# Performance work log

Hardware: AMD Instinct MI355X
Metric: run time of the kernel (lower is better)

The kernel has to match this reference:

```python
import jax, jax.numpy as jnp
import numpy as np

B, T, D, H = 2, 2048, 1024, 16
Dh = D // H
V = 32000  # vocab for kWTA potentials
KW_DECAY, KW_THR, K_WIN = 0.7, 1.0, 5
GAIN_UP, GAIN_DOWN = 1.5, 0.6
SPIKE_THR = 0.5


def setup_inputs() -> dict:
    key = jax.random.key(0)
    ks = jax.random.split(key, 10)
    x = jax.random.normal(ks[0], (B, T, D), dtype=jnp.float32)
    token_ids = jax.random.randint(ks[1], (B, T), 0, V)
    # xavier_uniform with gain 0.5 for square DxD weights
    bound = 0.5 * np.sqrt(6.0 / (D + D))
    def w(k):
        return jax.random.uniform(k, (D, D), dtype=jnp.float32, minval=-bound, maxval=bound)
    Wr, Wk, Wv, Wo = w(ks[2]), w(ks[3]), w(ks[4]), w(ks[5])
    bo = jnp.zeros((D,), dtype=jnp.float32)
    def tm(k):
        return jax.random.uniform(k, (1, 1, D), dtype=jnp.float32, minval=0.1, maxval=0.9)
    time_mix_k, time_mix_v, time_mix_r = tm(ks[6]), tm(ks[7]), tm(ks[8])
    return {"x": x, "token_ids": token_ids, "Wr": Wr, "Wk": Wk, "Wv": Wv,
            "Wo": Wo, "bo": bo, "time_mix_k": time_mix_k,
            "time_mix_v": time_mix_v, "time_mix_r": time_mix_r}


def kwta_gains(token_ids):
    """Sequential spiking k-WTA over the flattened token stream -> (V,) gains."""
    ids = token_ids.reshape(-1)
    def step(carry, tid):
        pot, spk = carry
        pot = pot * KW_DECAY
        pot = pot.at[tid].add(1.0)          # bincount of single token
        fired = pot >= KW_THR
        spk = spk + fired.astype(jnp.int32)
        pot = jnp.where(fired, pot - KW_THR, pot)  # soft reset
        return (pot, spk), None
    init = (jnp.zeros((V,), jnp.float32), jnp.zeros((V,), jnp.int32))
    (pot, spk), _ = jax.lax.scan(step, init, ids)
    values = spk.astype(jnp.float32) * 1e6 + pot
    topk_idx = jax.lax.top_k(values, K_WIN)[1]
    gains = jnp.where(spk > 0, GAIN_DOWN, 1.0).astype(jnp.float32)
    gains = gains.at[topk_idx].set(GAIN_UP)
    return gains


def spike_activation(x):
    # training-mode STE: hard spikes forward, clamp(1-|x-thr|,0,1) surrogate grad
    spikes = (x > SPIKE_THR).astype(x.dtype)
    ste = jnp.clip(1.0 - jnp.abs(x - SPIKE_THR), 0.0, 1.0)
    return spikes + ste - jax.lax.stop_gradient(ste)


def reference(x, token_ids, Wr, Wk, Wv, Wo, bo, time_mix_k, time_mix_v, time_mix_r):
    gains = jax.lax.stop_gradient(kwta_gains(token_ids))[:D]  # (D,)
    # token shift: prev_state starts as zeros
    prev_x = jnp.concatenate([jnp.zeros((B, 1, D), x.dtype), x[:, :-1]], axis=1)
    def mix(tm):
        m = tm.reshape(D) * gains               # adaptive time mixing with kWTA gains
        return m * x + (1.0 - m) * prev_x
    xr, xk, xv = mix(time_mix_r), mix(time_mix_k), mix(time_mix_v)
    r = xr @ Wr.T                                # [B,T,D]
    k = spike_activation(xk @ Wk.T)
    v = xv @ Wv.T
    def heads(t):
        return t.reshape(B, T, H, Dh).transpose(0, 2, 1, 3)  # [B,H,T,Dh]
    q_, k_, v_ = heads(r), heads(k), heads(v)
    # chunked_attention is an exact tiled full (non-causal) softmax attention
    scores = jnp.einsum('bhqd,bhkd->bhqk', q_, k_) * (1.0 / np.sqrt(Dh))
    attn = jax.nn.softmax(scores, axis=-1)
    out = jnp.einsum('bhqk,bhkd->bhqd', attn, v_)
    out = out.transpose(0, 2, 1, 3).reshape(B, T, D)
    out = jax.nn.sigmoid(r) * out                # receptance gating
    return out @ Wo.T + bo
```

## Files before the change

### kernel.cpp

```cpp
#include <hip/hip_runtime.h>
#include <stdint.h>

static constexpr int CB = 2, CT = 2048, CD = 1024, CH = 16, CDh = 64, CV = 32000;
static constexpr int CM = CB * CT;

typedef float f32x4 __attribute__((ext_vector_type(4)));
typedef float f32x16 __attribute__((ext_vector_type(16)));
typedef short s16x8 __attribute__((ext_vector_type(8)));
typedef unsigned u32x2 __attribute__((ext_vector_type(2)));

__device__ __forceinline__ unsigned short f2bf(float f) {
  unsigned u = __builtin_bit_cast(unsigned, f);
  unsigned r = 0x7FFFu + ((u >> 16) & 1u);
  return (unsigned short)((u + r) >> 16);
}
__device__ __forceinline__ float bf2f(unsigned short h) {
  unsigned u = ((unsigned)h) << 16;
  return __builtin_bit_cast(float, u);
}
__device__ __forceinline__ unsigned pkrh(float a, float b) {
  unsigned ua = __builtin_bit_cast(unsigned, a) + 0x8000u;
  unsigned ub = __builtin_bit_cast(unsigned, b) + 0x8000u;
  return __builtin_amdgcn_perm(ub, ua, 0x07060302);
}
__device__ __forceinline__ void lds_cp16(const void* g, void* l) {
  __builtin_amdgcn_global_load_lds(
      (const __attribute__((address_space(1))) unsigned*)g,
      (__attribute__((address_space(3))) unsigned*)l, 16, 0, 0);
}

__device__ __forceinline__ void chain5(unsigned n, unsigned& b0, unsigned& b1, unsigned& b2,
                                       unsigned& b3, unsigned& b4) {
  unsigned t;
  t = b0 > n ? b0 : n; n = b0 > n ? n : b0; b0 = t;
  t = b1 > n ? b1 : n; n = b1 > n ? n : b1; b1 = t;
  t = b2 > n ? b2 : n; n = b2 > n ? n : b2; b2 = t;
  t = b3 > n ? b3 : n; n = b3 > n ? n : b3; b3 = t;
  b4 = b4 > n ? b4 : n;
}

__global__ __launch_bounds__(1024) void nsr_gains(const int* __restrict__ ids,
                                                  int* __restrict__ bins,
                                                  float* __restrict__ gains) {
  __shared__ unsigned l5[5120];
  __shared__ unsigned w5[320];
  __shared__ unsigned fin[5];
  int tid = threadIdx.x;
  for (int i = tid; i < CV; i += 1024) bins[i] = 0;
  __syncthreads();
#pragma unroll
  for (int i = 0; i < 4; ++i) atomicAdd(&bins[ids[i * 1024 + tid]], 1);
  __syncthreads();
  unsigned b0 = 0, b1 = 0, b2 = 0, b3 = 0, b4 = 0;
  for (int i = tid; i < CV; i += 1024) {
    unsigned key = (((unsigned)bins[i]) << 15) | (unsigned)(32767 - i);
    chain5(key, b0, b1, b2, b3, b4);
  }
  l5[tid] = b0; l5[1024 + tid] = b1; l5[2048 + tid] = b2; l5[3072 + tid] = b3; l5[4096 + tid] = b4;
  __syncthreads();
  if (tid < 64) {
    unsigned c0 = 0, c1 = 0, c2 = 0, c3 = 0, c4 = 0;
    for (int i = tid; i < 5120; i += 64) chain5(l5[i], c0, c1, c2, c3, c4);
    w5[tid] = c0; w5[64 + tid] = c1; w5[128 + tid] = c2; w5[192 + tid] = c3; w5[256 + tid] = c4;
  }
  __syncthreads();
  if (tid == 0) {
    unsigned c0 = 0, c1 = 0, c2 = 0, c3 = 0, c4 = 0;
    for (int i = 0; i < 320; ++i) chain5(w5[i], c0, c1, c2, c3, c4);
    fin[0] = c0; fin[1] = c1; fin[2] = c2; fin[3] = c3; fin[4] = c4;
  }
  __syncthreads();
  {
    int cnt = bins[tid];
    float g = cnt > 0 ? 0.6f : 1.0f;
    unsigned key = (((unsigned)cnt) << 15) | (unsigned)(32767 - tid);
    if (key == fin[0] || key == fin[1] || key == fin[2] || key == fin[3] || key == fin[4])
      g = 1.5f;
    gains[tid] = g;
  }
}

__device__ __forceinline__ unsigned short mix1(float tm, float g, float xc, float px) {
  float m = tm * g;
  return f2bf(m * xc + (1.f - m) * px);
}

__global__ void nsr_cvtw_mix(const float* __restrict__ Wr, const float* __restrict__ Wk,
                             const float* __restrict__ Wv, const float* __restrict__ Wo,
                             unsigned short* __restrict__ dst, const float* __restrict__ x,
                             const float* __restrict__ gains, const float* __restrict__ tmr,
                             const float* __restrict__ tmk, const float* __restrict__ tmv,
                             unsigned short* __restrict__ xr, unsigned short* __restrict__ xk,
                             unsigned short* __restrict__ xv) {
  int bid = blockIdx.x;
  if (bid < 4096) {
    int i = bid * 256 + threadIdx.x;
    int which = i >> 18;
    int j = (i & 0x3FFFF) << 2;
    const float* s = which == 0 ? Wr : which == 1 ? Wk : which == 2 ? Wv : Wo;
    float4 v = *(const float4*)(s + j);
    ushort4 o = make_ushort4(f2bf(v.x), f2bf(v.y), f2bf(v.z), f2bf(v.w));
    *(ushort4*)(dst + (size_t)which * (CD * CD) + j) = o;
  } else {
    int i = (bid - 4096) * 256 + threadIdx.x;
    int m = i >> 8;
    int d = (i & 255) << 2;
    int t = m & (CT - 1);
    size_t base = (size_t)m * CD + d;
    float4 xc = *(const float4*)(x + base);
    float4 px = make_float4(0.f, 0.f, 0.f, 0.f);
    if (t > 0) px = *(const float4*)(x + base - CD);
    float4 g = *(const float4*)(gains + d);
    float4 ar = *(const float4*)(tmr + d);
    float4 ak = *(const float4*)(tmk + d);
    float4 av = *(const float4*)(tmv + d);
    *(ushort4*)(xr + base) = make_ushort4(mix1(ar.x, g.x, xc.x, px.x), mix1(ar.y, g.y, xc.y, px.y),
                                          mix1(ar.z, g.z, xc.z, px.z), mix1(ar.w, g.w, xc.w, px.w));
    *(ushort4*)(xk + base) = make_ushort4(mix1(ak.x, g.x, xc.x, px.x), mix1(ak.y, g.y, xc.y, px.y),
                                          mix1(ak.z, g.z, xc.z, px.z), mix1(ak.w, g.w, xc.w, px.w));
    *(ushort4*)(xv + base) = make_ushort4(mix1(av.x, g.x, xc.x, px.x), mix1(av.y, g.y, xc.y, px.y),
                                          mix1(av.z, g.z, xc.z, px.z), mix1(av.w, g.w, xc.w, px.w));
  }
}

__device__ __forceinline__ void swz_tiles(int bl, int& m0, int& n0) {
  int xcd = bl & 7, idx = bl >> 3;
  int mt8 = xcd * 4 + (idx & 3);
  int nt8 = idx >> 2;
  m0 = mt8 << 7;
  n0 = nt8 << 7;
}

__device__ __forceinline__ void gemm128(const unsigned short* __restrict__ A,
                                        const unsigned short* __restrict__ W, int m0, int n0,
                                        int Klen, int ld, int tid, f32x4 acc[4][4],
                                        unsigned short* As, unsigned short* Bs) {
  const f32x4 fz = {0.f, 0.f, 0.f, 0.f};
  int lane = tid & 63, w = tid >> 6;
  int wm = (w >> 1) << 6, wn = (w & 1) << 6;
  int l15 = lane & 15, quad = lane >> 4;
#pragma unroll
  for (int mt = 0; mt < 4; ++mt)
#pragma unroll
    for (int nt = 0; nt < 4; ++nt) acc[mt][nt] = fz;
  for (int k0 = 0; k0 < Klen; k0 += 32) {
#pragma unroll
    for (int i = 0; i < 2; ++i) {
      int chunk = i * 256 + tid;
      int r = chunk >> 2, cp = chunk & 3, c = cp ^ (r & 3);
      lds_cp16(A + (size_t)(m0 + r) * ld + k0 + c * 8, &As[(chunk & ~63) << 3]);
      lds_cp16(W + (size_t)(n0 + r) * ld + k0 + c * 8, &Bs[(chunk & ~63) << 3]);
    }
    __syncthreads();
    s16x8 af[4], bf[4];
#pragma unroll
    for (int mt = 0; mt < 4; ++mt) {
      int row = wm + mt * 16 + l15;
      af[mt] = *(const s16x8*)&As[row * 32 + ((quad ^ (row & 3)) << 3)];
    }
#pragma unroll
    for (int nt = 0; nt < 4; ++nt) {
      int row = wn + nt * 16 + l15;
      bf[nt] = *(const s16x8*)&Bs[row * 32 + ((quad ^ (row & 3)) << 3)];
    }
#pragma unroll
    for (int mt = 0; mt < 4; ++mt)
#pragma unroll
      for (int nt = 0; nt < 4; ++nt)
        acc[mt][nt] = __builtin_amdgcn_mfma_f32_16x16x32_bf16(af[mt], bf[nt], acc[mt][nt], 0, 0, 0);
    __syncthreads();
  }
}

__global__ __launch_bounds__(256) void nsr_proj(const unsigned short* __restrict__ xr,
                                                const unsigned short* __restrict__ xk,
                                                const unsigned short* __restrict__ xv,
                                                const unsigned short* __restrict__ Wb,
                                                unsigned short* __restrict__ r,
                                                unsigned short* __restrict__ k,
                                                unsigned short* __restrict__ vt) {
  __shared__ alignas(16) unsigned short As[128 * 32];
  __shared__ alignas(16) unsigned short Bs[128 * 32];
  __shared__ alignas(16) unsigned short vts[128 * 136];
  int bid = blockIdx.x;
  int which = bid >> 8;
  int m0, n0;
  swz_tiles(bid & 255, m0, n0);
  const unsigned short* A = which == 0 ? xr : which == 1 ? xk : xv;
  const unsigned short* W = Wb + (size_t)which * (CD * CD);
  f32x4 acc[4][4];
  gemm128(A, W, m0, n0, CD, CD, threadIdx.x, acc, As, Bs);
  int tid = threadIdx.x;
  int lane = tid & 63, w = tid >> 6;
  int wm = (w >> 1) << 6, wn = (w & 1) << 6;
  int l15 = lane & 15, quad = lane >> 4;
  if (which < 2) {
    unsigned short* out = which == 0 ? r : k;
#pragma unroll
    for (int mt = 0; mt < 4; ++mt)
#pragma unroll
      for (int nt = 0; nt < 4; ++nt)
#pragma unroll
        for (int rr = 0; rr < 4; ++rr) {
          int grow = m0 + wm + mt * 16 + quad * 4 + rr;
          int gcol = n0 + wn + nt * 16 + l15;
          float val = acc[mt][nt][rr];
          if (which == 1) val = val > 0.5f ? 1.0f : 0.0f;
          out[(size_t)grow * CD + gcol] = f2bf(val);
        }
  } else {
#pragma unroll
    for (int mt = 0; mt < 4; ++mt)
#pragma unroll
      for (int nt = 0; nt < 4; ++nt) {
        int gcl = wn + nt * 16 + l15;
        int gr = wm + mt * 16 + quad * 4;
        unsigned lo = pkrh(acc[mt][nt][0], acc[mt][nt][1]);
        unsigned hi = pkrh(acc[mt][nt][2], acc[mt][nt][3]);
        uint2 pk = make_uint2(lo, hi);
        *(uint2*)&vts[gcl * 136 + gr] = pk;
      }
    __syncthreads();
    int b2 = m0 >> 11, t0 = m0 & (CT - 1);
    int ch = tid & 15, dl2 = tid >> 4;
#pragma unroll
    for (int rr2 = 0; rr2 < 8; ++rr2) {
      int dloc = rr2 * 16 + dl2;
      int h = (n0 + dloc) >> 6, dl = (n0 + dloc) & 63;
      s16x8 val = *(const s16x8*)&vts[dloc * 136 + ch * 8];
      size_t ob = ((size_t)((b2 * CH + h) * CDh + dl)) * CT + t0 + ch * 8;
      *(s16x8*)(vt + ob) = val;
    }
  }
}

__global__ __launch_bounds__(512, 2) void nsr_attn(const unsigned short* __restrict__ rbf,
                                                   const unsigned short* __restrict__ kbf,
                                                   const unsigned short* __restrict__ vt,
                                                   unsigned short* __restrict__ gated) {
  __shared__ alignas(16) unsigned char smem[32768];
  __shared__ float denp[2][128];
  unsigned short* Ks = (unsigned short*)smem;
  unsigned short* Vs = (unsigned short*)(smem + 16384);
  float* Ored = (float*)smem;

  const f32x16 fz16 = {0.f, 0.f, 0.f, 0.f, 0.f, 0.f, 0.f, 0.f,
                       0.f, 0.f, 0.f, 0.f, 0.f, 0.f, 0.f, 0.f};
  const float EXSC = 0.125f * 1.44269504088896f;
  int bid = blockIdx.x;
  int b = bid & 1, hd = (bid >> 1) & 15, qt = bid >> 5;
  int tid = threadIdx.x, lane = tid & 63, w = tid >> 6;
  int l31 = lane & 31, hbit = lane >> 5;
  int qh = w & 3, kq2 = w >> 2;

  const unsigned short* qrow = rbf + (size_t)(b * CT + qt * 128 + qh * 32 + l31) * CD + hd * 64;
  s16x8 qfrag[4];
#pragma unroll
  for (int s4 = 0; s4 < 4; ++s4) {
    s16x8 qf = *(const s16x8*)(qrow + s4 * 16 + hbit * 8);
    unsigned* qd = (unsigned*)&qf;
#pragma unroll
    for (int j = 0; j < 4; ++j) {
      float lo = __builtin_bit_cast(float, qd[j] << 16) * EXSC;
      float hi = __builtin_bit_cast(float, qd[j] & 0xFFFF0000u) * EXSC;
      qd[j] = pkrh(lo, hi);
    }
    qfrag[s4] = qf;
  }

  const unsigned short* kap[2][4];
#pragma unroll
  for (int ktile = 0; ktile < 2; ++ktile) {
    int keyrow = kq2 * 64 + ktile * 32 + l31;
#pragma unroll
    for (int s4 = 0; s4 < 4; ++s4) {
      int cp = (s4 * 2 + hbit) ^ (keyrow & 7);
      kap[ktile][s4] = &Ks[keyrow * 64 + cp * 8];
    }
  }
  const unsigned short* vap[2][2][2];
#pragma unroll
  for (int ktile = 0; ktile < 2; ++ktile)
#pragma unroll
    for (int s = 0; s < 2; ++s)
#pragma unroll
      for (int dt = 0; dt < 2; ++dt) {
        int drow = dt * 32 + l31;
        int c = kq2 * 8 + ktile * 4 + s * 2 + hbit;
        int cp = (c & 8) | ((c ^ drow) & 7);
        vap[ktile][s][dt] = &Vs[drow * 128 + cp * 8];
      }

  const unsigned short* kgp[2];
  const unsigned short* vgp[2];
  unsigned short* ldk[2];
  unsigned short* ldv[2];
  {
    const unsigned short* kgbase = kbf + (size_t)(b * CT) * CD + hd * 64;
    const unsigned short* vgbase = vt + (size_t)((b * CH + hd) * CDh) * CT;
#pragma unroll
    for (int i = 0; i < 2; ++i) {
      int L = i * 512 + tid;
      int key = L >> 3, cpk = (L & 7) ^ (key & 7);
      kgp[i] = kgbase + (size_t)key * CD + cpk * 8;
      ldk[i] = &Ks[(L & ~63) << 3];
      int d = L >> 4, cp2 = L & 15, c2 = (cp2 & 8) | ((cp2 ^ d) & 7);
      vgp[i] = vgbase + (size_t)d * CT + c2 * 8;
      ldv[i] = &Vs[(L & ~63) << 3];
    }
  }

  f32x16 o_acc[2];
  o_acc[0] = fz16;
  o_acc[1] = fz16;
  float den0 = 0.f, den1 = 0.f;

  for (int kt = 0; kt < 16; ++kt) {
#pragma unroll
    for (int i = 0; i < 2; ++i) {
      lds_cp16(kgp[i], ldk[i]);
      lds_cp16(vgp[i], ldv[i]);
      kgp[i] += 128 * CD;
      vgp[i] += 128;
    }
    __syncthreads();

#pragma unroll
    for (int ktile = 0; ktile < 2; ++ktile) {
      f32x16 sc = fz16;
#pragma unroll
      for (int s4 = 0; s4 < 4; ++s4)
        sc = __builtin_amdgcn_mfma_f32_32x32x16_bf16(*(const s16x8*)kap[ktile][s4], qfrag[s4], sc,
                                                     0, 0, 0);
#pragma unroll
      for (int s = 0; s < 2; ++s) {
        int rb = 8 * s;
        float p0 = __builtin_amdgcn_exp2f(sc[rb + 0]);
        float p1 = __builtin_amdgcn_exp2f(sc[rb + 1]);
        float p2 = __builtin_amdgcn_exp2f(sc[rb + 2]);
        float p3 = __builtin_amdgcn_exp2f(sc[rb + 3]);
        float p4 = __builtin_amdgcn_exp2f(sc[rb + 4]);
        float p5 = __builtin_amdgcn_exp2f(sc[rb + 5]);
        float p6 = __builtin_amdgcn_exp2f(sc[rb + 6]);
        float p7 = __builtin_amdgcn_exp2f(sc[rb + 7]);
        den0 += (p0 + p1) + (p2 + p3);
        den1 += (p4 + p5) + (p6 + p7);
        unsigned P01 = pkrh(p0, p1), P23 = pkrh(p2, p3);
        unsigned P45 = pkrh(p4, p5), P67 = pkrh(p6, p7);
        unsigned br[4];
#if __has_builtin(__builtin_amdgcn_permlane32_swap)
        u32x2 sw0 = __builtin_amdgcn_permlane32_swap(P01, P45, false, false);
        u32x2 sw1 = __builtin_amdgcn_permlane32_swap(P23, P67, false, false);
        br[0] = sw0.x; br[2] = sw0.y;
        br[1] = sw1.x; br[3] = sw1.y;
#else
        unsigned send0 = hbit ? P01 : P45;
        unsigned send1 = hbit ? P23 : P67;
        unsigned recv0 = (unsigned)__shfl_xor((int)send0, 32);
        unsigned recv1 = (unsigned)__shfl_xor((int)send1, 32);
        br[0] = hbit ? recv0 : P01;
        br[1] = hbit ? recv1 : P23;
        br[2] = hbit ? P45 : recv0;
        br[3] = hbit ? P67 : recv1;
#endif
        s16x8 bfrag = __builtin_bit_cast(s16x8, *(const unsigned(*)[4])br);
        o_acc[0] = __builtin_amdgcn_mfma_f32_32x32x16_bf16(*(const s16x8*)vap[ktile][s][0], bfrag,
                                                           o_acc[0], 0, 0, 0);
        o_acc[1] = __builtin_amdgcn_mfma_f32_32x32x16_bf16(*(const s16x8*)vap[ktile][s][1], bfrag,
                                                           o_acc[1], 0, 0, 0);
      }
    }
    __syncthreads();
  }

  float den = den0 + den1;
  den += __shfl_xor(den, 32);
  if (hbit == 0) denp[kq2][qh * 32 + l31] = den;
  __syncthreads();
  float rinv = 1.0f / (denp[0][qh * 32 + l31] + denp[1][qh * 32 + l31]);

  if (kq2 == 1) {
#pragma unroll
    for (int dt = 0; dt < 2; ++dt)
#pragma unroll
      for (int rr = 0; rr < 16; ++rr) {
        int d = dt * 32 + (rr & 3) + 8 * (rr >> 2) + 4 * hbit;
        Ored[qh * 2048 + d * 32 + l31] = o_acc[dt][rr];
      }
  }
  __syncthreads();
  if (kq2 == 0) {
#pragma unroll
    for (int dt = 0; dt < 2; ++dt)
#pragma unroll
      for (int rr = 0; rr < 16; ++rr) {
        int d = dt * 32 + (rr & 3) + 8 * (rr >> 2) + 4 * hbit;
        int idx = qh * 2048 + d * 32 + l31;
        Ored[idx] = (o_acc[dt][rr] + Ored[idx]) * rinv;
      }
  }
  __syncthreads();

  int q = tid >> 2, dc = tid & 3;
  size_t grow = (size_t)(b * CT + qt * 128 + q) * CD + hd * 64 + dc * 16;
  s16x8 rv0 = *(const s16x8*)(rbf + grow);
  s16x8 rv1 = *(const s16x8*)(rbf + grow + 8);
  unsigned short outv[16];
#pragma unroll
  for (int i = 0; i < 16; ++i) {
    float o = Ored[(q >> 5) * 2048 + (dc * 16 + i) * 32 + (q & 31)];
    float rv = bf2f(i < 8 ? ((unsigned short*)&rv0)[i] : ((unsigned short*)&rv1)[i - 8]);
    float sig = 1.f / (1.f + __expf(-rv));
    outv[i] = f2bf(sig * o);
  }
  *(s16x8*)(gated + grow) = *(s16x8*)&outv[0];
  *(s16x8*)(gated + grow + 8) = *(s16x8*)&outv[8];
}

__global__ __launch_bounds__(256) void nsr_out(const unsigned short* __restrict__ gated,
                                               const unsigned short* __restrict__ Wo,
                                               const float* __restrict__ bo,
                                               float* __restrict__ out) {
  __shared__ alignas(16) unsigned short As[128 * 32];
  __shared__ alignas(16) unsigned short Bs[128 * 32];
  int m0, n0;
  swz_tiles(blockIdx.x, m0, n0);
  f32x4 acc[4][4];
  gemm128(gated, Wo, m0, n0, CD, CD, threadIdx.x, acc, As, Bs);
  int lane = threadIdx.x & 63, w = threadIdx.x >> 6;
  int wm = (w >> 1) << 6, wn = (w & 1) << 6;
  int l15 = lane & 15, quad = lane >> 4;
#pragma unroll
  for (int mt = 0; mt < 4; ++mt)
#pragma unroll
    for (int nt = 0; nt < 4; ++nt)
#pragma unroll
      for (int rr = 0; rr < 4; ++rr) {
        int grow = m0 + wm + mt * 16 + quad * 4 + rr;
        int gcol = n0 + wn + nt * 16 + l15;
        out[(size_t)grow * CD + gcol] = acc[mt][nt][rr] + bo[gcol];
      }
}

extern "C" void kernel_launch(void* const* d_in, const int* in_sizes, int n_in,
                              void* d_out, int out_size, void* d_ws, size_t ws_size,
                              hipStream_t stream) {
  const float* x = (const float*)d_in[0];
  const int* ids = (const int*)d_in[1];
  const float* Wr = (const float*)d_in[2];
  const float* Wk = (const float*)d_in[3];
  const float* Wv = (const float*)d_in[4];
  const float* Wo = (const float*)d_in[5];
  const float* bo = (const float*)d_in[6];
  const float* tmk = (const float*)d_in[7];
  const float* tmv = (const float*)d_in[8];
  const float* tmr = (const float*)d_in[9];

  char* ws = (char*)d_ws;
  size_t off = 0;
  int* bins = (int*)(ws + off); off += 131072;
  float* gains = (float*)(ws + off); off += 4096;
  unsigned short* Wb = (unsigned short*)(ws + off); off += (size_t)4 * CD * CD * 2;
  unsigned short* xr = (unsigned short*)(ws + off); off += (size_t)CM * CD * 2;
  unsigned short* xk = (unsigned short*)(ws + off); off += (size_t)CM * CD * 2;
  unsigned short* xv = (unsigned short*)(ws + off); off += (size_t)CM * CD * 2;
  unsigned short* rb = (unsigned short*)(ws + off); off += (size_t)CM * CD * 2;
  unsigned short* kb = (unsigned short*)(ws + off); off += (size_t)CM * CD * 2;
  unsigned short* vtb = (unsigned short*)(ws + off); off += (size_t)CM * CD * 2;
  unsigned short* gatedb = (unsigned short*)(ws + off); off += (size_t)CM * CD * 2;

  nsr_gains<<<1, 1024, 0, stream>>>(ids, bins, gains);
  nsr_cvtw_mix<<<8192, 256, 0, stream>>>(Wr, Wk, Wv, Wo, Wb, x, gains, tmr, tmk, tmv, xr, xk, xv);
  nsr_proj<<<768, 256, 0, stream>>>(xr, xk, xv, Wb, rb, kb, vtb);
  nsr_attn<<<512, 512, 0, stream>>>(rb, kb, vtb, gatedb);
  nsr_out<<<256, 256, 0, stream>>>(gatedb, Wb + (size_t)3 * CD * CD, bo, (float*)d_out);
}
```

Baseline: 241.0 us.

## Double-buffer LDS tiles in projection and output GEMMs with one barrier per step

Replaces the single-buffered GEMM main loop with a double-buffered version. The loop issues async global-to-LDS copies for the next K slice into the alternate buffer before running the MFMAs on the current slice, and drops the trailing barrier so each iteration has one sync. In the projection kernel the transpose scratch now aliases the GEMM buffers, with an added barrier before reuse, so total LDS per block goes down. The aim is to hide global load latency behind MFMA work and cut barrier stalls. The cost is extra address registers and a dependence on the barrier draining the async copies.

```diff
diff --git a/kernel.cpp b/kernel.cpp
--- a/kernel.cpp
+++ b/kernel.cpp
@@ -131,10 +131,10 @@
   n0 = nt8 << 7;
 }
 
-__device__ __forceinline__ void gemm128(const unsigned short* __restrict__ A,
-                                        const unsigned short* __restrict__ W, int m0, int n0,
-                                        int Klen, int ld, int tid, f32x4 acc[4][4],
-                                        unsigned short* As, unsigned short* Bs) {
+__device__ __forceinline__ void gemm128_db(const unsigned short* __restrict__ A,
+                                           const unsigned short* __restrict__ W, int m0, int n0,
+                                           int Klen, int ld, int tid, f32x4 acc[4][4],
+                                           unsigned short* S) {
   const f32x4 fz = {0.f, 0.f, 0.f, 0.f};
   int lane = tid & 63, w = tid >> 6;
   int wm = (w >> 1) << 6, wn = (w & 1) << 6;
@@ -143,32 +143,49 @@
   for (int mt = 0; mt < 4; ++mt)
 #pragma unroll
     for (int nt = 0; nt < 4; ++nt) acc[mt][nt] = fz;
+
+  int r0 = tid >> 2, cp0 = tid & 3, c0 = cp0 ^ (r0 & 3);
+  int r1 = (256 + tid) >> 2, cp1 = tid & 3, c1 = cp1 ^ (r1 & 3);
+  const unsigned short* a0 = A + (size_t)(m0 + r0) * ld + c0 * 8;
+  const unsigned short* a1 = A + (size_t)(m0 + r1) * ld + c1 * 8;
+  const unsigned short* w0 = W + (size_t)(n0 + r0) * ld + c0 * 8;
+  const unsigned short* w1 = W + (size_t)(n0 + r1) * ld + c1 * 8;
+  int ldso0 = (tid & ~63) << 3;
+  int ldso1 = ((256 + tid) & ~63) << 3;
+
+  lds_cp16(a0, &S[ldso0]);
+  lds_cp16(w0, &S[4096 + ldso0]);
+  lds_cp16(a1, &S[ldso1]);
+  lds_cp16(w1, &S[4096 + ldso1]);
+
   for (int k0 = 0; k0 < Klen; k0 += 32) {
-#pragma unroll
-    for (int i = 0; i < 2; ++i) {
-      int chunk = i * 256 + tid;
-      int r = chunk >> 2, cp = chunk & 3, c = cp ^ (r & 3);
-      lds_cp16(A + (size_t)(m0 + r) * ld + k0 + c * 8, &As[(chunk & ~63) << 3]);
-      lds_cp16(W + (size_t)(n0 + r) * ld + k0 + c * 8, &Bs[(chunk & ~63) << 3]);
-    }
+    int cur = (k0 >> 5) & 1;
+    unsigned short* Sc = S + cur * 8192;
     __syncthreads();
+    if (k0 + 32 < Klen) {
+      unsigned short* Sn = S + (cur ^ 1) * 8192;
+      int kn = k0 + 32;
+      lds_cp16(a0 + kn, &Sn[ldso0]);
+      lds_cp16(w0 + kn, &Sn[4096 + ldso0]);
+      lds_cp16(a1 + kn, &Sn[ldso1]);
+      lds_cp16(w1 + kn, &Sn[4096 + ldso1]);
+    }
     s16x8 af[4], bf[4];
 #pragma unroll
     for (int mt = 0; mt < 4; ++mt) {
       int row = wm + mt * 16 + l15;
-      af[mt] = *(const s16x8*)&As[row * 32 + ((quad ^ (row & 3)) << 3)];
+      af[mt] = *(const s16x8*)&Sc[row * 32 + ((quad ^ (row & 3)) << 3)];
     }
 #pragma unroll
     for (int nt = 0; nt < 4; ++nt) {
       int row = wn + nt * 16 + l15;
-      bf[nt] = *(const s16x8*)&Bs[row * 32 + ((quad ^ (row & 3)) << 3)];
+      bf[nt] = *(const s16x8*)&Sc[4096 + row * 32 + ((quad ^ (row & 3)) << 3)];
     }
 #pragma unroll
     for (int mt = 0; mt < 4; ++mt)
 #pragma unroll
       for (int nt = 0; nt < 4; ++nt)
         acc[mt][nt] = __builtin_amdgcn_mfma_f32_16x16x32_bf16(af[mt], bf[nt], acc[mt][nt], 0, 0, 0);
-    __syncthreads();
   }
 }
 
@@ -179,9 +196,7 @@
                                                 unsigned short* __restrict__ r,
                                                 unsigned short* __restrict__ k,
                                                 unsigned short* __restrict__ vt) {
-  __shared__ alignas(16) unsigned short As[128 * 32];
-  __shared__ alignas(16) unsigned short Bs[128 * 32];
-  __shared__ alignas(16) unsigned short vts[128 * 136];
+  __shared__ alignas(16) unsigned short smem[128 * 136];
   int bid = blockIdx.x;
   int which = bid >> 8;
   int m0, n0;
@@ -189,7 +204,7 @@
   const unsigned short* A = which == 0 ? xr : which == 1 ? xk : xv;
   const unsigned short* W = Wb + (size_t)which * (CD * CD);
   f32x4 acc[4][4];
-  gemm128(A, W, m0, n0, CD, CD, threadIdx.x, acc, As, Bs);
+  gemm128_db(A, W, m0, n0, CD, CD, threadIdx.x, acc, smem);
   int tid = threadIdx.x;
   int lane = tid & 63, w = tid >> 6;
   int wm = (w >> 1) << 6, wn = (w & 1) << 6;
@@ -209,6 +224,8 @@
           out[(size_t)grow * CD + gcol] = f2bf(val);
         }
   } else {
+    unsigned short* vts = smem;
+    __syncthreads();
 #pragma unroll
     for (int mt = 0; mt < 4; ++mt)
 #pragma unroll
@@ -421,12 +438,11 @@
                                                const unsigned short* __restrict__ Wo,
                                                const float* __restrict__ bo,
                                                float* __restrict__ out) {
-  __shared__ alignas(16) unsigned short As[128 * 32];
-  __shared__ alignas(16) unsigned short Bs[128 * 32];
+  __shared__ alignas(16) unsigned short smem[4 * 4096];
   int m0, n0;
   swz_tiles(blockIdx.x, m0, n0);
   f32x4 acc[4][4];
-  gemm128(gated, Wo, m0, n0, CD, CD, threadIdx.x, acc, As, Bs);
+  gemm128_db(gated, Wo, m0, n0, CD, CD, threadIdx.x, acc, smem);
   int lane = threadIdx.x & 63, w = threadIdx.x >> 6;
   int wm = (w >> 1) << 6, wn = (w & 1) << 6;
   int l15 = lane & 15, quad = lane >> 4;
```

After: 225.4 us. 1.07x faster.
